# Performance work log

Measured on AMD Instinct MI355X. Metric: run time of the kernel, lower is better.

The kernel has to match this reference:

```python
import jax, jax.numpy as jnp
import numpy as np

B, S, E, H = 4, 2048, 1024, 16
D = E // H  # head dim = 64


def setup_inputs() -> dict:
    key = jax.random.key(0)
    ks = jax.random.split(key, 5)
    s = 0.02
    return {
        "x": jax.random.normal(ks[0], (B, S, E), dtype=jnp.float32),
        "Wq": jax.random.normal(ks[1], (E, E), dtype=jnp.float32) * s,
        "Wk": jax.random.normal(ks[2], (E, E), dtype=jnp.float32) * s,
        "Wv": jax.random.normal(ks[3], (E, E), dtype=jnp.float32) * s,
        "Wo": jax.random.normal(ks[4], (E, E), dtype=jnp.float32) * s,
        "bo": jnp.zeros((E,), dtype=jnp.float32),
    }


def reference(x, Wq, Wk, Wv, Wo, bo):
    b, s, e = x.shape
    h, d = H, e // H
    # QKV projections -> [b, h, s, d]
    q = (x @ Wq).reshape(b, s, h, d).transpose(0, 2, 1, 3)
    k = (x @ Wk).reshape(b, s, h, d).transpose(0, 2, 1, 3)
    v = (x @ Wv).reshape(b, s, h, d).transpose(0, 2, 1, 3)
    # scores [b, h, s, s], causal mask with -inf, scaled softmax
    a = jnp.einsum('bhqd,bhkd->bhqk', q, k)
    causal = jnp.tril(jnp.ones((s, s), dtype=bool))  # True where allowed
    a = jnp.where(causal, a, -jnp.inf) / jnp.sqrt(jnp.asarray(d, x.dtype))
    a = jax.nn.softmax(a, axis=-1)
    # dropout p=0.0 (identity in eval)
    y = jnp.einsum('bhqk,bhkd->bhqd', a, v)
    y = y.transpose(0, 2, 1, 3).reshape(b, s, e)
    return y @ Wo + bo
```

## Files before the change

kernel.cpp:

```cpp
#include <hip/hip_runtime.h>

typedef __bf16 bf16x8 __attribute__((ext_vector_type(8)));
typedef float f32x4 __attribute__((ext_vector_type(4)));
typedef float f32x16 __attribute__((ext_vector_type(16)));
typedef unsigned short u16x8 __attribute__((ext_vector_type(8)));
typedef unsigned int u32x4 __attribute__((ext_vector_type(4)));
typedef unsigned int u32x2v __attribute__((ext_vector_type(2)));

#define S_LEN 2048
#define NHEAD 16
#define HDIM  64
#define EMB   1024

__device__ __forceinline__ ushort f2b(float v) {
  union { float f; unsigned u; } x; x.f = v;
  unsigned r = (x.u + 0x7fffu + ((x.u >> 16) & 1u)) >> 16;
  return (ushort)r;
}

__device__ __forceinline__ unsigned pk2(float lo, float hi) {
  union { float f; unsigned u; } a, b; a.f = lo; b.f = hi;
  return (b.u & 0xffff0000u) | (a.u >> 16);
}

typedef const __attribute__((address_space(1))) unsigned int* gp1_t;
typedef __attribute__((address_space(3))) unsigned int* lp3_t;
__device__ __forceinline__ void gld16(const ushort* g, const ushort* l) {
  __builtin_amdgcn_global_load_lds((gp1_t)(unsigned long long)(uintptr_t)g,
                                   (lp3_t)(unsigned int)(uintptr_t)l, 16, 0, 0);
}

__device__ __forceinline__ void barf() {
  asm volatile("" ::: "memory");
  __builtin_amdgcn_s_barrier();
  asm volatile("" ::: "memory");
}

__global__ __launch_bounds__(256) void prep_kernel(
    const float* __restrict__ x, const float* __restrict__ W0,
    const float* __restrict__ W1, const float* __restrict__ W2,
    const float* __restrict__ W3, ushort* __restrict__ xb,
    ushort* __restrict__ Wt0, ushort* __restrict__ Wt1,
    ushort* __restrict__ Wt2, ushort* __restrict__ Wt3, float scale0) {
  const int z = blockIdx.z;
  if (z == 4) {
    size_t base = ((size_t)(blockIdx.y * 32 + blockIdx.x)) * 8192 + threadIdx.x * 4;
#pragma unroll
    for (int i = 0; i < 8; ++i) {
      float4 v = *(const float4*)(x + base + i * 1024);
      ushort4 o;
      o.x = f2b(v.x); o.y = f2b(v.y); o.z = f2b(v.z); o.w = f2b(v.w);
      *(ushort4*)(xb + base + i * 1024) = o;
    }
    return;
  }
  __shared__ float t[32][33];
  const float* W = z == 0 ? W0 : (z == 1 ? W1 : (z == 2 ? W2 : W3));
  ushort* Wt = z == 0 ? Wt0 : (z == 1 ? Wt1 : (z == 2 ? Wt2 : Wt3));
  const float scale = z == 0 ? scale0 : 1.0f;
  int k0 = blockIdx.x * 32, n0 = blockIdx.y * 32;
  int c = threadIdx.x & 31, r0 = threadIdx.x >> 5;
#pragma unroll
  for (int i = 0; i < 4; ++i) {
    int r = r0 + i * 8;
    t[r][c] = W[(size_t)(k0 + r) * EMB + n0 + c];
  }
  __syncthreads();
#pragma unroll
  for (int i = 0; i < 4; ++i) {
    int r = r0 + i * 8;
    Wt[(size_t)(n0 + r) * EMB + k0 + c] = f2b(t[c][r] * scale);
  }
}

template <int EPI>
__global__ __launch_bounds__(512, 2) void gemm8_kernel(
    const ushort* __restrict__ A, const ushort* __restrict__ Bt,
    ushort* __restrict__ outQ, ushort* __restrict__ outK, ushort* __restrict__ outVt,
    float* __restrict__ outF, const float* __restrict__ bias) {
  __shared__ ushort lds8[73728];
  const int tid = threadIdx.x;
  const int wave = tid >> 6, lane = tid & 63, ln = lane & 15, quad = lane >> 4;
  const int wm = wave >> 2, wn = wave & 3;
  const long m0 = (long)blockIdx.x * 128, n0 = (long)blockIdx.y * 256;
  constexpr int K = EMB, KT = K / 64;

  const int srow = tid >> 3;
  const int scol = ((tid & 7) ^ (srow & 7)) * 8;
  const ushort* srcA = A + (m0 + srow) * (long)K + scol;
  const ushort* srcB = Bt + (n0 + srow) * (long)K + scol;

#define STG_A(t, s)                                                            \
  do {                                                                         \
    gld16(srcA + (t) * 64,               lds8 + (s) * 8192 + tid * 8);         \
    gld16(srcA + (t) * 64 + 64 * K,      lds8 + (s) * 8192 + 4096 + tid * 8);  \
  } while (0)
#define STG_B(t, s)                                                            \
  do {                                                                         \
    gld16(srcB + (t) * 64,               lds8 + 24576 + (s) * 16384 + tid * 8);         \
    gld16(srcB + (t) * 64 + 64 * K,      lds8 + 24576 + (s) * 16384 + 4096 + tid * 8);  \
    gld16(srcB + (t) * 64 + 128 * K,     lds8 + 24576 + (s) * 16384 + 8192 + tid * 8);  \
    gld16(srcB + (t) * 64 + 192 * K,     lds8 + 24576 + (s) * 16384 + 12288 + tid * 8); \
  } while (0)

  const int sw = (ln & 7) * 8;

#define RD_A(F, kk, s)                                                         \
  do {                                                                         \
    const ushort* p_ = lds8 + (s) * 8192 + (wm * 64 + ln) * 64 +               \
                       (((kk) * 32 + quad * 8) ^ sw);                          \
    F[0] = *(const bf16x8*)p_;                                                 \
    F[1] = *(const bf16x8*)(p_ + 1024);                                        \
    F[2] = *(const bf16x8*)(p_ + 2048);                                        \
    F[3] = *(const bf16x8*)(p_ + 3072);                                        \
  } while (0)
#define RD_B(F, kk, s)                                                         \
  do {                                                                         \
    const ushort* p_ = lds8 + 24576 + (s) * 16384 + (wn * 64 + ln) * 64 +      \
                       (((kk) * 32 + quad * 8) ^ sw);                          \
    F[0] = *(const bf16x8*)p_;                                                 \
    F[1] = *(const bf16x8*)(p_ + 1024);                                        \
    F[2] = *(const bf16x8*)(p_ + 2048);                                        \
    F[3] = *(const bf16x8*)(p_ + 3072);                                        \
  } while (0)

#define MM16(AF, BF)                                                           \
  do {                                                                         \
    __builtin_amdgcn_s_setprio(1);                                             \
    _Pragma("unroll") for (int mt = 0; mt < 4; ++mt)                           \
        _Pragma("unroll") for (int nt = 0; nt < 4; ++nt)                       \
            acc[mt][nt] = __builtin_amdgcn_mfma_f32_16x16x32_bf16(             \
                AF[mt], BF[nt], acc[mt][nt], 0, 0, 0);                         \
    __builtin_amdgcn_s_setprio(0);                                             \
  } while (0)

  f32x4 acc[4][4] = {};
  bf16x8 afP[4], bfP[4], afN[4], bfN[4];

  STG_A(0, 0); STG_B(0, 0);
  STG_A(1, 1); STG_B(1, 1);
  asm volatile("s_waitcnt vmcnt(6)" ::: "memory");
  barf();
  RD_A(afP, 0, 0); RD_B(bfP, 0, 0);

#define TILE_FULL(t, s, s1, s2)                                                \
  do {                                                                         \
    STG_A((t) + 2, s2);                                                        \
    RD_A(afN, 1, s); RD_B(bfN, 1, s);                                          \
    MM16(afP, bfP);                                                            \
    STG_B((t) + 2, s2);                                                        \
    asm volatile("s_waitcnt vmcnt(6) lgkmcnt(0)" ::: "memory");                \
    barf();                                                                    \
    RD_A(afP, 0, s1); RD_B(bfP, 0, s1);                                        \
    MM16(afN, bfN);                                                            \
  } while (0)

  for (int th = 0; th < 12; th += 3) {
    TILE_FULL(th, 0, 1, 2);
    TILE_FULL(th + 1, 1, 2, 0);
    TILE_FULL(th + 2, 2, 0, 1);
  }
  TILE_FULL(12, 0, 1, 2);
  TILE_FULL(13, 1, 2, 0);
  RD_A(afN, 1, 2); RD_B(bfN, 1, 2);
  MM16(afP, bfP);
  asm volatile("s_waitcnt vmcnt(0) lgkmcnt(0)" ::: "memory");
  barf();
  RD_A(afP, 0, 0); RD_B(bfP, 0, 0);
  MM16(afN, bfN);
  RD_A(afN, 1, 0); RD_B(bfN, 1, 0);
  MM16(afP, bfP);
  MM16(afN, bfN);

  if (EPI == 0) {
    const int sel = (int)(n0 >> 10);
    if (sel == 2) {
#pragma unroll
      for (int mt = 0; mt < 4; ++mt) {
        const long mbase = m0 + wm * 64 + mt * 16 + quad * 4;
        const long bb = mbase >> 11, s = mbase & 2047;
#pragma unroll
        for (int nt = 0; nt < 4; ++nt) {
          const int nn = (int)((n0 & 1023) + wn * 64 + nt * 16 + ln);
          const int h = nn >> 6, d = nn & 63;
          uint2 val;
          val.x = (unsigned)f2b(acc[mt][nt][0]) | ((unsigned)f2b(acc[mt][nt][1]) << 16);
          val.y = (unsigned)f2b(acc[mt][nt][2]) | ((unsigned)f2b(acc[mt][nt][3]) << 16);
          *(uint2*)(outVt + (((bb * NHEAD + h) * (long)HDIM + d) * S_LEN) + s) = val;
        }
      }
    } else {
      ushort* dst = sel == 0 ? outQ : outK;
#pragma unroll
      for (int mt = 0; mt < 4; ++mt) {
#pragma unroll
        for (int nt = 0; nt < 4; ++nt) {
          const int nn = (int)((n0 & 1023) + wn * 64 + nt * 16 + ln);
          const int h = nn >> 6, d = nn & 63;
#pragma unroll
          for (int r = 0; r < 4; ++r) {
            const long m = m0 + wm * 64 + mt * 16 + quad * 4 + r;
            const long bb = m >> 11, s = m & 2047;
            dst[(((bb * NHEAD + h) * S_LEN) + s) * HDIM + d] = f2b(acc[mt][nt][r]);
          }
        }
      }
    }
  } else {
#pragma unroll
    for (int mt = 0; mt < 4; ++mt) {
#pragma unroll
      for (int nt = 0; nt < 4; ++nt) {
        const long n = n0 + wn * 64 + nt * 16 + ln;
        const float bv = bias[n];
#pragma unroll
        for (int r = 0; r < 4; ++r) {
          const long m = m0 + wm * 64 + mt * 16 + quad * 4 + r;
          outF[m * (long)EMB + n] = acc[mt][nt][r] + bv;
        }
      }
    }
  }
#undef TILE_FULL
#undef MM16
#undef RD_B
#undef RD_A
#undef STG_B
#undef STG_A
}

__global__ __launch_bounds__(256, 3) void attn_kernel(const ushort* __restrict__ Q,
                                                      const ushort* __restrict__ Kg,
                                                      const ushort* __restrict__ Vt,
                                                      ushort* __restrict__ Y) {
  __shared__ alignas(16) ushort Ks[2][4096];
  __shared__ alignas(16) ushort Vs[2][4096];
  const int tid = threadIdx.x;
  const int wave = tid >> 6, lane = tid & 63;
  const int l31 = lane & 31, hi = lane >> 5;
  const int bh = blockIdx.x;
  const int qb = 15 - (int)blockIdx.y;
  const int q0 = qb * 128;
  const size_t base = (size_t)bh * S_LEN * HDIM;
  const int ntiles = 2 * qb + 2;

  const u16x8 ob = {0x3F80, 0x3F80, 0x3F80, 0x3F80, 0x3F80, 0x3F80, 0x3F80, 0x3F80};
  const bf16x8 ones = __builtin_bit_cast(bf16x8, ob);

  bf16x8 qf[4];
#pragma unroll
  for (int dsub = 0; dsub < 4; ++dsub)
    qf[dsub] = *(const bf16x8*)(Q + base + (size_t)(q0 + wave * 32 + l31) * HDIM +
                                dsub * 16 + hi * 8);

  f32x16 acc0 = {}, acc1 = {}, accl = {};

  const int srow = tid >> 3;
  const int scc  = ((tid & 7) ^ (srow & 7)) * 8;
  const ushort* KgS = Kg + base + (size_t)srow * HDIM + scc;
  const ushort* VgS = Vt + base + (size_t)srow * S_LEN + scc;

  {
    gld16(KgS,                       &Ks[0][0] + tid * 8);
    gld16(KgS + 32 * HDIM,           &Ks[0][0] + 2048 + tid * 8);
    gld16(VgS,                       &Vs[0][0] + tid * 8);
    gld16(VgS + 32 * (size_t)S_LEN,  &Vs[0][0] + 2048 + tid * 8);
  }
  __syncthreads();

  const int swL = (lane & 7) * 8;
  const int qbase = q0 + wave * 32;

  for (int kt = 0; kt < ntiles; ++kt) {
    const int cur = kt & 1;
    const int k0 = kt * 64;
    if (kt + 1 < ntiles) {
      const int nb = cur ^ 1;
      const size_t k1 = (size_t)(k0 + 64);
      gld16(KgS + k1 * HDIM,                  &Ks[nb][0] + tid * 8);
      gld16(KgS + (k1 + 32) * HDIM,           &Ks[nb][0] + 2048 + tid * 8);
      gld16(VgS + k1,                         &Vs[nb][0] + tid * 8);
      gld16(VgS + 32 * (size_t)S_LEN + k1,    &Vs[nb][0] + 2048 + tid * 8);
    }
    const ushort* Kc = &Ks[cur][0];
    const ushort* Vc = &Vs[cur][0];

    if (k0 < qbase + 32) {
      f32x16 sT0 = {}, sT1 = {};
#pragma unroll
      for (int dsub = 0; dsub < 4; ++dsub) {
        const int c = (dsub * 16 + hi * 8) ^ swL;
        bf16x8 kf0 = *(const bf16x8*)(Kc + l31 * 64 + c);
        bf16x8 kf1 = *(const bf16x8*)(Kc + (32 + l31) * 64 + c);
        sT0 = __builtin_amdgcn_mfma_f32_32x32x16_bf16(kf0, qf[dsub], sT0, 0, 0, 0);
        sT1 = __builtin_amdgcn_mfma_f32_32x32x16_bf16(kf1, qf[dsub], sT1, 0, 0, 0);
      }

      if (k0 + 63 > qbase) {
        const int rowq = qbase + l31;
#pragma unroll
        for (int r = 0; r < 16; ++r) {
          const int key = k0 + ((r & 3) + 8 * (r >> 2)) + 4 * hi;
          if (key > rowq) sT0[r] = -3.0e38f;
          if (key + 32 > rowq) sT1[r] = -3.0e38f;
        }
      }

      unsigned pw0[8], pw1[8];
#pragma unroll
      for (int i = 0; i < 8; ++i) {
        pw0[i] = pk2(__builtin_amdgcn_exp2f(sT0[2 * i]),
                     __builtin_amdgcn_exp2f(sT0[2 * i + 1]));
        pw1[i] = pk2(__builtin_amdgcn_exp2f(sT1[2 * i]),
                     __builtin_amdgcn_exp2f(sT1[2 * i + 1]));
      }

#define KEYBLK(PW, KSQ0)                                                       \
  do {                                                                         \
    u32x2v r02 = __builtin_amdgcn_permlane32_swap(PW[0], PW[2], false, false); \
    u32x2v r13 = __builtin_amdgcn_permlane32_swap(PW[1], PW[3], false, false); \
    u32x2v r46 = __builtin_amdgcn_permlane32_swap(PW[4], PW[6], false, false); \
    u32x2v r57 = __builtin_amdgcn_permlane32_swap(PW[5], PW[7], false, false); \
    u32x4 fwA, fwB;                                                            \
    fwA[0] = r02[0]; fwA[1] = r13[0]; fwA[2] = r02[1]; fwA[3] = r13[1];        \
    fwB[0] = r46[0]; fwB[1] = r57[0]; fwB[2] = r46[1]; fwB[3] = r57[1];        \
    bf16x8 paA = __builtin_bit_cast(bf16x8, fwA);                              \
    bf16x8 paB = __builtin_bit_cast(bf16x8, fwB);                              \
    accl = __builtin_amdgcn_mfma_f32_32x32x16_bf16(paA, ones, accl, 0, 0, 0);  \
    accl = __builtin_amdgcn_mfma_f32_32x32x16_bf16(paB, ones, accl, 0, 0, 0);  \
    {                                                                          \
      const int vcA = (((KSQ0)) * 16 + hi * 8) ^ swL;                          \
      bf16x8 va0 = *(const bf16x8*)(Vc + l31 * 64 + vcA);                      \
      bf16x8 va1 = *(const bf16x8*)(Vc + (32 + l31) * 64 + vcA);               \
      acc0 = __builtin_amdgcn_mfma_f32_32x32x16_bf16(paA, va0, acc0, 0, 0, 0); \
      acc1 = __builtin_amdgcn_mfma_f32_32x32x16_bf16(paA, va1, acc1, 0, 0, 0); \
      const int vcB = (((KSQ0) + 1) * 16 + hi * 8) ^ swL;                      \
      bf16x8 vb0 = *(const bf16x8*)(Vc + l31 * 64 + vcB);                      \
      bf16x8 vb1 = *(const bf16x8*)(Vc + (32 + l31) * 64 + vcB);               \
      acc0 = __builtin_amdgcn_mfma_f32_32x32x16_bf16(paB, vb0, acc0, 0, 0, 0); \
      acc1 = __builtin_amdgcn_mfma_f32_32x32x16_bf16(paB, vb1, acc1, 0, 0, 0); \
    }                                                                          \
  } while (0)

      KEYBLK(pw0, 0);
      KEYBLK(pw1, 2);
#undef KEYBLK
    }
    __syncthreads();
  }

  const long b = bh >> 4;
  const int h = bh & 15;
#pragma unroll
  for (int r = 0; r < 16; ++r) {
    const float inv = 1.0f / accl[r];
    const int qq = q0 + wave * 32 + ((r & 3) + 8 * (r >> 2)) + 4 * hi;
    ushort* yp = Y + (((b * S_LEN + qq) * NHEAD) + h) * HDIM;
    yp[l31]      = f2b(acc0[r] * inv);
    yp[32 + l31] = f2b(acc1[r] * inv);
  }
}

extern "C" void kernel_launch(void* const* d_in, const int* in_sizes, int n_in,
                              void* d_out, int out_size, void* d_ws, size_t ws_size,
                              hipStream_t stream) {
  const float* x  = (const float*)d_in[0];
  const float* Wq = (const float*)d_in[1];
  const float* Wk = (const float*)d_in[2];
  const float* Wv = (const float*)d_in[3];
  const float* Wo = (const float*)d_in[4];
  const float* bo = (const float*)d_in[5];
  float* out = (float*)d_out;

  const size_t XE = (size_t)8192 * EMB;
  ushort* ws    = (ushort*)d_ws;
  ushort* xb    = ws;
  ushort* Wtqkv = xb + XE;
  ushort* Wto   = Wtqkv + 3 * 1048576;
  ushort* Qb    = Wto + 1048576;
  ushort* Kb    = Qb + XE;
  ushort* Vtb   = Kb + XE;
  ushort* Yb    = xb;

  const float SCALE_Q = 1.4426950408889634f / 8.0f;

  prep_kernel<<<dim3(32, 32, 5), 256, 0, stream>>>(
      x, Wq, Wk, Wv, Wo, xb, Wtqkv, Wtqkv + 1048576, Wtqkv + 2097152, Wto, SCALE_Q);

  gemm8_kernel<0><<<dim3(64, 12), 512, 0, stream>>>(xb, Wtqkv, Qb, Kb, Vtb,
                                                    nullptr, nullptr);
  attn_kernel<<<dim3(64, 16), 256, 0, stream>>>(Qb, Kb, Vtb, Yb);
  gemm8_kernel<1><<<dim3(64, 4), 512, 0, stream>>>(Yb, Wto, nullptr, nullptr,
                                                   nullptr, out, bo);
}
```

Baseline: 225.5 us.

## Triple-buffer K/V tiles with fine-grained vmcnt waits and MFMA priority

Expands the attention kernel's K/V shared-memory staging from double to triple buffering, so tile kt+2 is loading while tile kt is computed. The full __syncthreads is replaced by explicit s_waitcnt vmcnt(4) waits plus a barrier, which wait only for the older tile's loads. MFMA sections are also wrapped in s_setprio to favour the matrix-issuing waves. LDS use rises from 32KB to 48KB per block, which may reduce occupancy against launch_bounds(256,3).

```diff
diff --git a/kernel.cpp b/kernel.cpp
--- a/kernel.cpp
+++ b/kernel.cpp
@@ -233,8 +233,8 @@
                                                       const ushort* __restrict__ Kg,
                                                       const ushort* __restrict__ Vt,
                                                       ushort* __restrict__ Y) {
-  __shared__ alignas(16) ushort Ks[2][4096];
-  __shared__ alignas(16) ushort Vs[2][4096];
+  __shared__ alignas(16) ushort Ks[3][4096];
+  __shared__ alignas(16) ushort Vs[3][4096];
   const int tid = threadIdx.x;
   const int wave = tid >> 6, lane = tid & 63;
   const int l31 = lane & 31, hi = lane >> 5;
@@ -260,33 +260,35 @@
   const ushort* KgS = Kg + base + (size_t)srow * HDIM + scc;
   const ushort* VgS = Vt + base + (size_t)srow * S_LEN + scc;
 
-  {
-    gld16(KgS,                       &Ks[0][0] + tid * 8);
-    gld16(KgS + 32 * HDIM,           &Ks[0][0] + 2048 + tid * 8);
-    gld16(VgS,                       &Vs[0][0] + tid * 8);
-    gld16(VgS + 32 * (size_t)S_LEN,  &Vs[0][0] + 2048 + tid * 8);
-  }
-  __syncthreads();
+#define STAGE(t, s)                                                            \
+  do {                                                                         \
+    const size_t kk_ = (size_t)(t) * 64;                                       \
+    gld16(KgS + kk_ * HDIM,               &Ks[s][0] + tid * 8);                \
+    gld16(KgS + (kk_ + 32) * HDIM,        &Ks[s][0] + 2048 + tid * 8);         \
+    gld16(VgS + kk_,                      &Vs[s][0] + tid * 8);                \
+    gld16(VgS + 32 * (size_t)S_LEN + kk_, &Vs[s][0] + 2048 + tid * 8);         \
+  } while (0)
+
+  STAGE(0, 0);
+  STAGE(1, 1);
+  asm volatile("s_waitcnt vmcnt(4)" ::: "memory");
+  barf();
 
   const int swL = (lane & 7) * 8;
   const int qbase = q0 + wave * 32;
+  int sc = 0, sn = 1, ss = 2;
 
   for (int kt = 0; kt < ntiles; ++kt) {
-    const int cur = kt & 1;
     const int k0 = kt * 64;
-    if (kt + 1 < ntiles) {
-      const int nb = cur ^ 1;
-      const size_t k1 = (size_t)(k0 + 64);
-      gld16(KgS + k1 * HDIM,                  &Ks[nb][0] + tid * 8);
-      gld16(KgS + (k1 + 32) * HDIM,           &Ks[nb][0] + 2048 + tid * 8);
-      gld16(VgS + k1,                         &Vs[nb][0] + tid * 8);
-      gld16(VgS + 32 * (size_t)S_LEN + k1,    &Vs[nb][0] + 2048 + tid * 8);
-    }
-    const ushort* Kc = &Ks[cur][0];
-    const ushort* Vc = &Vs[cur][0];
+    const bool do_stage = (kt + 2 < ntiles);
+    if (do_stage) STAGE(kt + 2, ss);
+
+    const ushort* Kc = &Ks[sc][0];
+    const ushort* Vc = &Vs[sc][0];
 
     if (k0 < qbase + 32) {
       f32x16 sT0 = {}, sT1 = {};
+      __builtin_amdgcn_s_setprio(1);
 #pragma unroll
       for (int dsub = 0; dsub < 4; ++dsub) {
         const int c = (dsub * 16 + hi * 8) ^ swL;
@@ -295,6 +297,7 @@
         sT0 = __builtin_amdgcn_mfma_f32_32x32x16_bf16(kf0, qf[dsub], sT0, 0, 0, 0);
         sT1 = __builtin_amdgcn_mfma_f32_32x32x16_bf16(kf1, qf[dsub], sT1, 0, 0, 0);
       }
+      __builtin_amdgcn_s_setprio(0);
 
       if (k0 + 63 > qbase) {
         const int rowq = qbase + l31;
@@ -326,6 +329,7 @@
     fwB[0] = r46[0]; fwB[1] = r57[0]; fwB[2] = r46[1]; fwB[3] = r57[1];        \
     bf16x8 paA = __builtin_bit_cast(bf16x8, fwA);                              \
     bf16x8 paB = __builtin_bit_cast(bf16x8, fwB);                              \
+    __builtin_amdgcn_s_setprio(1);                                             \
     accl = __builtin_amdgcn_mfma_f32_32x32x16_bf16(paA, ones, accl, 0, 0, 0);  \
     accl = __builtin_amdgcn_mfma_f32_32x32x16_bf16(paB, ones, accl, 0, 0, 0);  \
     {                                                                          \
@@ -340,14 +344,25 @@
       acc0 = __builtin_amdgcn_mfma_f32_32x32x16_bf16(paB, vb0, acc0, 0, 0, 0); \
       acc1 = __builtin_amdgcn_mfma_f32_32x32x16_bf16(paB, vb1, acc1, 0, 0, 0); \
     }                                                                          \
+    __builtin_amdgcn_s_setprio(0);                                             \
   } while (0)
 
       KEYBLK(pw0, 0);
       KEYBLK(pw1, 2);
 #undef KEYBLK
     }
-    __syncthreads();
-  }
+
+    if (kt + 1 < ntiles) {
+      if (do_stage) {
+        asm volatile("s_waitcnt vmcnt(4) lgkmcnt(0)" ::: "memory");
+      } else {
+        asm volatile("s_waitcnt vmcnt(0) lgkmcnt(0)" ::: "memory");
+      }
+      barf();
+    }
+    const int t_ = sc; sc = sn; sn = ss; ss = t_;
+  }
+#undef STAGE
 
   const long b = bh >> 4;
   const int h = bh & 15;
```

After: 229.7 us. Within noise of the previous version (+1.9%).
